# Kernel optimization log

Hardware: AMD Instinct MI355X
Metric: run time of the kernel (lower is better)

## Reference

```python
import jax, jax.numpy as jnp
import numpy as np

N_NODES, N_EDGES, N_FEAT = 50000, 500000, 128
HID, LAT, N_GRAPHS = 256, 64, 512
HEADS, DH = 8, 32  # GAT: 8 heads x 32 = 256
EPS = 1e-5


def _seg_softmax(logits, seg, num):
    m = jax.ops.segment_max(logits, seg, num_segments=num)
    m = jnp.where(jnp.isfinite(m), m, 0.0)
    e = jnp.exp(logits - m[seg])
    s = jax.ops.segment_sum(e, seg, num_segments=num)
    return e / jnp.maximum(s[seg], 1e-16)


def _bn(h, g, b):  # BatchNorm1d, batch statistics
    mu = h.mean(0)
    var = h.var(0)
    return (h - mu) * jax.lax.rsqrt(var + EPS) * g + b


def _ln(h, g, b):
    mu = h.mean(-1, keepdims=True)
    var = h.var(-1, keepdims=True)
    return (h - mu) * jax.lax.rsqrt(var + EPS) * g + b


def setup_inputs() -> dict:
    key = jax.random.key(0)
    ks = iter(jax.random.split(key, 40))
    f = lambda *s: jax.random.normal(next(ks), s, dtype=jnp.float32) * 0.05
    inp = {
        'x': jax.random.normal(next(ks), (N_NODES, N_FEAT), dtype=jnp.float32),
        'W_emb': f(N_FEAT, HID), 'b_emb': f(HID),
        'W_gcn': f(HID, HID), 'b_gcn': f(HID),
        'W_gat': f(HID, HID), 'a_src': f(HEADS, DH), 'a_dst': f(HEADS, DH), 'b_gat': f(HID),
        'W_l': f(HID, HID), 'b_l': f(HID), 'W_r': f(HID, HID),
        'bn_gamma': jnp.ones((3, HID), jnp.float32), 'bn_beta': jnp.zeros((3, HID), jnp.float32),
        'Wg1': f(HID, HID // 2), 'bg1': f(HID // 2), 'Wg2': f(HID // 2, 1), 'bg2': f(1),
        'Wm1': f(HID, HID), 'bm1': f(HID), 'ln_m_g': jnp.ones(HID, jnp.float32), 'ln_m_b': jnp.zeros(HID, jnp.float32),
        'Wm2': f(HID, LAT), 'bm2': f(LAT),
        'Wv1': f(HID, HID), 'bv1': f(HID), 'ln_v_g': jnp.ones(HID, jnp.float32), 'ln_v_b': jnp.zeros(HID, jnp.float32),
        'Wv2': f(HID, LAT), 'bv2': f(LAT),
        'edge_index': jax.random.randint(next(ks), (2, N_EDGES), 0, N_NODES, dtype=jnp.int64),
        'batch': jnp.sort(jax.random.randint(next(ks), (N_NODES,), 0, N_GRAPHS, dtype=jnp.int64)),
    }
    return inp


def _forward(x, W_emb, b_emb, W_gcn, b_gcn, W_gat, a_src, a_dst, b_gat,
             W_l, b_l, W_r, bn_gamma, bn_beta, Wg1, bg1, Wg2, bg2,
             Wm1, bm1, ln_m_g, ln_m_b, Wm2, bm2, Wv1, bv1, ln_v_g, ln_v_b, Wv2, bv2,
             edge_index, batch):
    N = x.shape[0]
    loops = jnp.arange(N)
    src_sl = jnp.concatenate([edge_index[0], loops])  # with self-loops (GCN/GAT)
    dst_sl = jnp.concatenate([edge_index[1], loops])

    h = x @ W_emb + b_emb  # [N, HID]

    # --- layer 0: GCNConv ---
    deg = jax.ops.segment_sum(jnp.ones_like(dst_sl, dtype=h.dtype), dst_sl, num_segments=N)
    dis = jax.lax.rsqrt(deg)
    norm = dis[src_sl] * dis[dst_sl]  # [E+N]
    xt = h @ W_gcn
    out = jax.ops.segment_sum(xt[src_sl] * norm[:, None], dst_sl, num_segments=N) + b_gcn
    out = jax.nn.relu(_bn(out, bn_gamma[0], bn_beta[0]))
    h = h + out

    # --- layer 1: GATConv (8 heads, concat) ---
    xt = (h @ W_gat).reshape(N, HEADS, DH)
    al_src = (xt * a_src).sum(-1)  # [N, H]
    al_dst = (xt * a_dst).sum(-1)
    logits = jax.nn.leaky_relu(al_src[src_sl] + al_dst[dst_sl], 0.2)  # [E+N, H]
    alpha = _seg_softmax(logits, dst_sl, N)
    out = jax.ops.segment_sum(xt[src_sl] * alpha[:, :, None], dst_sl, num_segments=N)
    out = out.reshape(N, HID) + b_gat
    out = jax.nn.relu(_bn(out, bn_gamma[1], bn_beta[1]))
    h = h + out

    # --- layer 2: SAGEConv (mean aggregation, no self-loops) ---
    src, dst = edge_index[0], edge_index[1]
    cnt = jax.ops.segment_sum(jnp.ones_like(dst, dtype=h.dtype), dst, num_segments=N)
    nb_mean = jax.ops.segment_sum(h[src], dst, num_segments=N) / jnp.maximum(cnt, 1.0)[:, None]
    out = nb_mean @ W_l + b_l + h @ W_r
    out = jax.nn.relu(_bn(out, bn_gamma[2], bn_beta[2]))
    h = h + out

    # --- GlobalAttention pooling ---
    gate = (jax.nn.relu(h @ Wg1 + bg1) @ Wg2 + bg2)[:, 0]  # [N]
    w = _seg_softmax(gate, batch, N_GRAPHS)
    h_graph = jax.ops.segment_sum(h * w[:, None], batch, num_segments=N_GRAPHS)  # [G, HID]

    mu = jax.nn.relu(_ln(h_graph @ Wm1 + bm1, ln_m_g, ln_m_b)) @ Wm2 + bm2
    logvar = jax.nn.relu(_ln(h_graph @ Wv1 + bv1, ln_v_g, ln_v_b)) @ Wv2 + bv2
    return mu, logvar


def reference(x, W_emb, b_emb, W_gcn, b_gcn, W_gat, a_src, a_dst, b_gat,
              W_l, b_l, W_r, bn_gamma, bn_beta, Wg1, bg1, Wg2, bg2,
              Wm1, bm1, ln_m_g, ln_m_b, Wm2, bm2, Wv1, bv1, ln_v_g, ln_v_b, Wv2, bv2,
              edge_index, batch):
    return _forward(x, W_emb, b_emb, W_gcn, b_gcn, W_gat, a_src, a_dst, b_gat,
                    W_l, b_l, W_r, bn_gamma, bn_beta, Wg1, bg1, Wg2, bg2,
                    Wm1, bm1, ln_m_g, ln_m_b, Wm2, bm2, Wv1, bv1, ln_v_g, ln_v_b, Wv2, bv2,
                    edge_index, batch)
```

## Files before the change

### kernel.cpp

```cpp
#include <hip/hip_runtime.h>
#include <cstdint>
#include <cstddef>

#define N_NODES 50000
#define N_EDGES 500000
#define NG 512
#define HID 256
#define EPS 1e-5f
#define SCB 49

typedef __attribute__((ext_vector_type(8))) __bf16 bf16x8;
typedef __attribute__((ext_vector_type(8))) ushort u16x8;
typedef __attribute__((ext_vector_type(4))) float f32x4;

__device__ __forceinline__ ushort f2bf(float f) {
  uint32_t u = __float_as_uint(f);
  uint32_t r = (u + 0x7fffu + ((u >> 16) & 1u)) >> 16;
  return (ushort)r;
}
__device__ __forceinline__ float bfu(ushort u) { return __uint_as_float(((uint32_t)u) << 16); }
__device__ __forceinline__ float4 bf4(ushort4 u) {
  return make_float4(bfu(u.x), bfu(u.y), bfu(u.z), bfu(u.w));
}

__global__ void k_csr_count(const int* __restrict__ ei, int* __restrict__ cnt) {
  int e = blockIdx.x * 256 + threadIdx.x;
  if (e < N_EDGES) atomicAdd(&cnt[ei[N_EDGES + e]], 1);
}

__global__ void k_scan_part(const int* __restrict__ cnt, int* __restrict__ psum) {
  __shared__ int red[256];
  int tid = threadIdx.x;
  int i0 = blockIdx.x * 1024 + tid * 4;
  int s = 0;
  if (i0 + 4 <= N_NODES) {
    int4 v = *reinterpret_cast<const int4*>(cnt + i0);
    s = v.x + v.y + v.z + v.w;
  } else {
    for (int k = 0; k < 4; k++)
      if (i0 + k < N_NODES) s += cnt[i0 + k];
  }
  red[tid] = s;
  __syncthreads();
  for (int o = 128; o > 0; o >>= 1) {
    if (tid < o) red[tid] += red[tid + o];
    __syncthreads();
  }
  if (tid == 0) psum[blockIdx.x] = red[0];
}

__global__ void k_scan_top(const int* __restrict__ psum, int* __restrict__ boff,
                           int* __restrict__ row_ptr) {
  int t = threadIdx.x;
  int v = (t < SCB) ? psum[t] : 0;
  int own = v;
  for (int o = 1; o < 64; o <<= 1) {
    int u = __shfl_up(v, o);
    if (t >= o) v += u;
  }
  if (t < SCB) boff[t] = v - own;
  if (t == 63) row_ptr[N_NODES] = v;
}

__global__ void k_scan_out(const int* __restrict__ cnt, const int* __restrict__ boff,
                           int* __restrict__ row_ptr, float* __restrict__ dis) {
  __shared__ int ps[256];
  int tid = threadIdx.x;
  int i0 = blockIdx.x * 1024 + tid * 4;
  int v[4];
#pragma unroll
  for (int k = 0; k < 4; k++) v[k] = (i0 + k < N_NODES) ? cnt[i0 + k] : 0;
  int s = v[0] + v[1] + v[2] + v[3];
  ps[tid] = s;
  __syncthreads();
  for (int o = 1; o < 256; o <<= 1) {
    int add = (tid >= o) ? ps[tid - o] : 0;
    __syncthreads();
    ps[tid] += add;
    __syncthreads();
  }
  int run = boff[blockIdx.x] + ((tid > 0) ? ps[tid - 1] : 0);
#pragma unroll
  for (int k = 0; k < 4; k++) {
    if (i0 + k < N_NODES) {
      row_ptr[i0 + k] = run;
      dis[i0 + k] = rsqrtf((float)v[k] + 1.0f);
      run += v[k];
    }
  }
}

__global__ void k_csr_fill(const int* __restrict__ ei, const int* __restrict__ row_ptr,
                           int* __restrict__ fill, int* __restrict__ col_src) {
  int e = blockIdx.x * 256 + threadIdx.x;
  if (e >= N_EDGES) return;
  int s = ei[e], d = ei[N_EDGES + e];
  int pos = row_ptr[d] + atomicAdd(&fill[d], 1);
  col_src[pos] = s;
}

struct WtArgs {
  const float* src[6];
  ushort* dst[6];
  int K[6];
  int C[6];
  int off[6];
};

__global__ void k_wt_all(WtArgs a) {
  int b = blockIdx.x;
  int ji = 0;
#pragma unroll
  for (int t = 1; t < 6; t++)
    if (b >= a.off[t]) ji = t;
  int K = a.K[ji], C = a.C[ji];
  int i = (b - a.off[ji]) * 256 + threadIdx.x;
  int c = i / K, k = i - c * K;
  a.dst[ji][i] = f2bf(a.src[ji][k * C + c]);
}

template <int K, int C, bool DUAL, bool AFP32, bool GATE, bool GATAL, bool BNF>
__global__ __launch_bounds__(512) void k_mgemm(
    const void* __restrict__ A1v, const ushort* __restrict__ W1t,
    const ushort* __restrict__ A2, const ushort* __restrict__ W2t,
    const float* __restrict__ bias, ushort* __restrict__ out_bf,
    const float* __restrict__ gw, const float* __restrict__ gb,
    float* __restrict__ gate, const float* __restrict__ asv,
    const float* __restrict__ adv, float* __restrict__ als,
    float* __restrict__ ald, const float* __restrict__ scsh,
    ushort* __restrict__ hbuf, int M, int relu) {
  constexpr int KS = K / 32;
  constexpr int CHK = K / 8;
  constexpr int NPAN = C / 64;
  constexpr int NISS = (64 * CHK) / 512;
  constexpr int NTOT = NPAN * (DUAL ? 2 : 1);
  constexpr int PELEM = 64 * K;
  __shared__ ushort wlds[2 * PELEM];
  const int tid = threadIdx.x;
  const int lane = tid & 63;
  const int wid = tid >> 6;
  const int r16 = lane & 15;
  const int kg = lane >> 4;
  const int rbase = blockIdx.x * 128 + wid * 16;

  const bool avalid = (rbase + r16) < M;
  int arow = rbase + r16;
  if (arow >= M) arow = M - 1;

  bf16x8 af[KS], af2[KS];
  if constexpr (BNF) {
    const ushort* xp = (const ushort*)A1v + (size_t)arow * K + kg * 8;
    ushort* hp = hbuf + (size_t)arow * K + kg * 8;
#pragma unroll
    for (int ks = 0; ks < KS; ks++) {
      int col = kg * 8 + ks * 32;
      u16x8 xv = *reinterpret_cast<const u16x8*>(xp + ks * 32);
      u16x8 hv = *reinterpret_cast<const u16x8*>(hp + ks * 32);
      float4 sc0 = *reinterpret_cast<const float4*>(scsh + col);
      float4 sc1 = *reinterpret_cast<const float4*>(scsh + col + 4);
      float4 sh0 = *reinterpret_cast<const float4*>(scsh + 256 + col);
      float4 sh1 = *reinterpret_cast<const float4*>(scsh + 256 + col + 4);
      float scv[8] = {sc0.x, sc0.y, sc0.z, sc0.w, sc1.x, sc1.y, sc1.z, sc1.w};
      float shv[8] = {sh0.x, sh0.y, sh0.z, sh0.w, sh1.x, sh1.y, sh1.z, sh1.w};
      union { u16x8 u; bf16x8 b; } cv;
#pragma unroll
      for (int j = 0; j < 8; j++) {
        float v = fmaf(bfu(xv[j]), scv[j], shv[j]);
        float hn = bfu(hv[j]) + fmaxf(v, 0.f);
        cv.u[j] = f2bf(hn);
      }
      af[ks] = cv.b;
      if (avalid) *reinterpret_cast<u16x8*>(hp + ks * 32) = cv.u;
    }
  } else if constexpr (AFP32) {
    const float* ap = (const float*)A1v + (size_t)arow * K + kg * 8;
#pragma unroll
    for (int ks = 0; ks < KS; ks++) {
      float4 lo = *reinterpret_cast<const float4*>(ap + ks * 32);
      float4 hi = *reinterpret_cast<const float4*>(ap + ks * 32 + 4);
      union { u16x8 u; bf16x8 b; } cv;
      cv.u = (u16x8){f2bf(lo.x), f2bf(lo.y), f2bf(lo.z), f2bf(lo.w),
                     f2bf(hi.x), f2bf(hi.y), f2bf(hi.z), f2bf(hi.w)};
      af[ks] = cv.b;
    }
  } else {
    const ushort* ap = (const ushort*)A1v + (size_t)arow * K + kg * 8;
#pragma unroll
    for (int ks = 0; ks < KS; ks++)
      af[ks] = *reinterpret_cast<const bf16x8*>(ap + ks * 32);
  }
  if constexpr (DUAL) {
    const ushort* ap = A2 + (size_t)arow * K + kg * 8;
#pragma unroll
    for (int ks = 0; ks < KS; ks++)
      af2[ks] = *reinterpret_cast<const bf16x8*>(ap + ks * 32);
  }

  float greg[4] = {0.f, 0.f, 0.f, 0.f};
  f32x4 acc[4];

#define STAGE_ASYNC(WSRC, PAN, BUF)                                            \
  {                                                                            \
    const ushort* base_ = (WSRC) + (size_t)((PAN) * 64) * K;                   \
    _Pragma("unroll") for (int j = 0; j < NISS; j++) {                         \
      int p_ = j * 512 + tid;                                                  \
      int c_ = p_ / CHK, jj_ = p_ % CHK;                                       \
      const ushort* g_ = base_ + c_ * K + (jj_ ^ (c_ & 7)) * 8;                \
      ushort* l_ = &wlds[(BUF) * PELEM + (j * 512 + wid * 64) * 8];            \
      __builtin_amdgcn_global_load_lds(                                        \
          (const __attribute__((address_space(1))) void*)(g_),                 \
          (__attribute__((address_space(3))) void*)(l_), 16, 0, 0);            \
    }                                                                          \
  }

#define COMPUTE(AF, BUF)                                                       \
  {                                                                            \
    const ushort* wb_ = &wlds[(BUF) * PELEM];                                  \
    _Pragma("unroll") for (int ct = 0; ct < 4; ct++) {                         \
      bf16x8 wf[KS];                                                           \
      int colr = ct * 16 + r16;                                                \
      _Pragma("unroll") for (int ks = 0; ks < KS; ks++) {                      \
        int slot = colr * CHK + ((ks * 4 + kg) ^ (r16 & 7));                   \
        wf[ks] = *reinterpret_cast<const bf16x8*>(&wb_[slot * 8]);             \
      }                                                                        \
      _Pragma("unroll") for (int ks = 0; ks < KS; ks++)                        \
        acc[ct] = __builtin_amdgcn_mfma_f32_16x16x32_bf16((AF)[ks], wf[ks],    \
                                                          acc[ct], 0, 0, 0);   \
    }                                                                          \
  }

  STAGE_ASYNC(W1t, 0, 0);
  __syncthreads();

#pragma unroll
  for (int q = 0; q < NTOT; q++) {
    const int pan = DUAL ? (q >> 1) : q;
    const int pass = DUAL ? (q & 1) : 0;
    const int cur = q & 1;
    const int c0 = pan * 64;
    if (pass == 0) {
#pragma unroll
      for (int ct = 0; ct < 4; ct++) acc[ct] = (f32x4){0.f, 0.f, 0.f, 0.f};
    }
    if (q + 1 < NTOT) {
      const int npan = DUAL ? ((q + 1) >> 1) : (q + 1);
      const ushort* Wq = (DUAL && ((q + 1) & 1)) ? W2t : W1t;
      STAGE_ASYNC(Wq, npan, cur ^ 1);
    }
    if (DUAL && pass) {
      COMPUTE(af2, cur);
    } else {
      COMPUTE(af, cur);
    }
    if (pass == (DUAL ? 1 : 0)) {
      if constexpr (GATE) {
#pragma unroll
        for (int ct = 0; ct < 4; ct++) {
          int col = c0 + ct * 16 + r16;
          float bv = bias[col];
          float wv = gw[col];
#pragma unroll
          for (int i = 0; i < 4; i++) {
            float v = fmaxf(acc[ct][i] + bv, 0.f);
            greg[i] = fmaf(v, wv, greg[i]);
          }
        }
      } else {
#pragma unroll
        for (int ct = 0; ct < 4; ct++) {
          int col = c0 + ct * 16 + r16;
          float bv = bias ? bias[col] : 0.f;
#pragma unroll
          for (int i = 0; i < 4; i++) {
            int row = rbase + kg * 4 + i;
            if (row < M) {
              float v = acc[ct][i] + bv;
              if (relu) v = fmaxf(v, 0.f);
              out_bf[(size_t)row * C + col] = f2bf(v);
            }
          }
        }
      }
      if constexpr (GATAL) {
        float ps_[2][4], pd_[2][4];
#pragma unroll
        for (int h2 = 0; h2 < 2; h2++)
#pragma unroll
          for (int i = 0; i < 4; i++) { ps_[h2][i] = 0.f; pd_[h2][i] = 0.f; }
#pragma unroll
        for (int ct = 0; ct < 4; ct++) {
          int col = c0 + ct * 16 + r16;
          float as_ = asv[col], ad_ = adv[col];
          int h2 = ct >> 1;
#pragma unroll
          for (int i = 0; i < 4; i++) {
            ps_[h2][i] = fmaf(acc[ct][i], as_, ps_[h2][i]);
            pd_[h2][i] = fmaf(acc[ct][i], ad_, pd_[h2][i]);
          }
        }
#pragma unroll
        for (int h2 = 0; h2 < 2; h2++)
#pragma unroll
          for (int i = 0; i < 4; i++) {
#pragma unroll
            for (int o = 1; o < 16; o <<= 1) {
              ps_[h2][i] += __shfl_xor(ps_[h2][i], o);
              pd_[h2][i] += __shfl_xor(pd_[h2][i], o);
            }
          }
        if (r16 == 0) {
#pragma unroll
          for (int i = 0; i < 4; i++) {
            int row = rbase + kg * 4 + i;
            if (row < M) {
              als[row * 8 + pan * 2 + 0] = ps_[0][i];
              ald[row * 8 + pan * 2 + 0] = pd_[0][i];
              als[row * 8 + pan * 2 + 1] = ps_[1][i];
              ald[row * 8 + pan * 2 + 1] = pd_[1][i];
            }
          }
        }
      }
    }
    __syncthreads();
  }

  if constexpr (GATE) {
#pragma unroll
    for (int i = 0; i < 4; i++) {
#pragma unroll
      for (int o = 1; o < 16; o <<= 1) greg[i] += __shfl_xor(greg[i], o);
    }
    if (r16 == 0) {
      float b0 = gb[0];
#pragma unroll
      for (int i = 0; i < 4; i++) {
        int row = rbase + kg * 4 + i;
        if (row < M) gate[row] = greg[i] + b0;
      }
    }
  }
#undef STAGE_ASYNC
#undef COMPUTE
}

__global__ void k_gcn_agg(const ushort* __restrict__ xt, const float* __restrict__ dis,
                          const int* __restrict__ row_ptr, const int* __restrict__ col_src,
                          const float* __restrict__ b_gcn, ushort* __restrict__ outb) {
  int node = blockIdx.x * 4 + (threadIdx.x >> 6);
  if (node >= N_NODES) return;
  int lane = threadIdx.x & 63;
  int half = lane >> 5;
  int c0 = (lane & 31) * 8;
  float di = dis[node];
  float acc[8];
#pragma unroll
  for (int j = 0; j < 8; j++) acc[j] = 0.f;
  int b = row_ptr[node], e = row_ptr[node + 1];
  int g0 = b;
  for (; g0 + 8 <= e; g0 += 8) {
    int i0 = g0 + half * 4;
    int s0 = col_src[i0], s1 = col_src[i0 + 1], s2 = col_src[i0 + 2], s3 = col_src[i0 + 3];
    float w0 = di * dis[s0], w1 = di * dis[s1], w2 = di * dis[s2], w3 = di * dis[s3];
    u16x8 u0 = *reinterpret_cast<const u16x8*>(xt + (size_t)s0 * HID + c0);
    u16x8 u1 = *reinterpret_cast<const u16x8*>(xt + (size_t)s1 * HID + c0);
    u16x8 u2 = *reinterpret_cast<const u16x8*>(xt + (size_t)s2 * HID + c0);
    u16x8 u3 = *reinterpret_cast<const u16x8*>(xt + (size_t)s3 * HID + c0);
#pragma unroll
    for (int j = 0; j < 8; j++) {
      acc[j] = fmaf(bfu(u0[j]), w0, acc[j]);
      acc[j] = fmaf(bfu(u1[j]), w1, acc[j]);
      acc[j] = fmaf(bfu(u2[j]), w2, acc[j]);
      acc[j] = fmaf(bfu(u3[j]), w3, acc[j]);
    }
  }
  for (; g0 + 4 <= e; g0 += 4) {
    int i0 = g0 + half * 2;
    int s0 = col_src[i0], s1 = col_src[i0 + 1];
    float w0 = di * dis[s0], w1 = di * dis[s1];
    u16x8 u0 = *reinterpret_cast<const u16x8*>(xt + (size_t)s0 * HID + c0);
    u16x8 u1 = *reinterpret_cast<const u16x8*>(xt + (size_t)s1 * HID + c0);
#pragma unroll
    for (int j = 0; j < 8; j++) {
      acc[j] = fmaf(bfu(u0[j]), w0, acc[j]);
      acc[j] = fmaf(bfu(u1[j]), w1, acc[j]);
    }
  }
  {
    int i0 = g0 + half * 2;
    int s0 = 0, s1 = 0;
    float w0 = 0.f, w1 = 0.f;
    if (i0 < e) { s0 = col_src[i0]; w0 = di * dis[s0]; }
    if (i0 + 1 < e) { s1 = col_src[i0 + 1]; w1 = di * dis[s1]; }
    u16x8 u0 = *reinterpret_cast<const u16x8*>(xt + (size_t)s0 * HID + c0);
    u16x8 u1 = *reinterpret_cast<const u16x8*>(xt + (size_t)s1 * HID + c0);
#pragma unroll
    for (int j = 0; j < 8; j++) {
      acc[j] = fmaf(bfu(u0[j]), w0, acc[j]);
      acc[j] = fmaf(bfu(u1[j]), w1, acc[j]);
    }
  }
#pragma unroll
  for (int j = 0; j < 8; j++) acc[j] += __shfl_xor(acc[j], 32);
  if (!half) {
    u16x8 un = *reinterpret_cast<const u16x8*>(xt + (size_t)node * HID + c0);
    float w0 = di * di;
    u16x8 r;
#pragma unroll
    for (int j = 0; j < 8; j++) {
      float v = fmaf(bfu(un[j]), w0, acc[j]) + b_gcn[c0 + j];
      r[j] = f2bf(v);
    }
    *reinterpret_cast<u16x8*>(outb + (size_t)node * HID + c0) = r;
  }
}

__device__ __forceinline__ float leaky02(float x) { return x > 0.f ? x : 0.2f * x; }

__global__ void k_gat_agg(const ushort* __restrict__ xt, const float* __restrict__ alsrc,
                          const float* __restrict__ aldst, const int* __restrict__ row_ptr,
                          const int* __restrict__ col_src, const float* __restrict__ b_gat,
                          ushort* __restrict__ outb) {
  int node = blockIdx.x * 4 + (threadIdx.x >> 6);
  if (node >= N_NODES) return;
  int lane = threadIdx.x & 63;
  int half = lane >> 5;
  int l32 = lane & 31;
  int c0 = l32 * 8;
  int hh = l32 >> 2;
  float ad = aldst[node * 8 + hh];
  float acc[8];
#pragma unroll
  for (int j = 0; j < 8; j++) acc[j] = 0.f;
  float s = 0.f;
  int b = row_ptr[node], e = row_ptr[node + 1];
  int g0 = b;
  for (; g0 + 8 <= e; g0 += 8) {
    int i0 = g0 + half * 4;
    int s0 = col_src[i0], s1 = col_src[i0 + 1], s2 = col_src[i0 + 2], s3 = col_src[i0 + 3];
    float g0v = alsrc[s0 * 8 + hh], g1v = alsrc[s1 * 8 + hh];
    float g2v = alsrc[s2 * 8 + hh], g3v = alsrc[s3 * 8 + hh];
    u16x8 u0 = *reinterpret_cast<const u16x8*>(xt + (size_t)s0 * HID + c0);
    u16x8 u1 = *reinterpret_cast<const u16x8*>(xt + (size_t)s1 * HID + c0);
    u16x8 u2 = *reinterpret_cast<const u16x8*>(xt + (size_t)s2 * HID + c0);
    u16x8 u3 = *reinterpret_cast<const u16x8*>(xt + (size_t)s3 * HID + c0);
    float a0 = __expf(leaky02(g0v + ad));
    float a1 = __expf(leaky02(g1v + ad));
    float a2 = __expf(leaky02(g2v + ad));
    float a3 = __expf(leaky02(g3v + ad));
    s += a0 + a1 + a2 + a3;
#pragma unroll
    for (int j = 0; j < 8; j++) {
      acc[j] = fmaf(bfu(u0[j]), a0, acc[j]);
      acc[j] = fmaf(bfu(u1[j]), a1, acc[j]);
      acc[j] = fmaf(bfu(u2[j]), a2, acc[j]);
      acc[j] = fmaf(bfu(u3[j]), a3, acc[j]);
    }
  }
  for (; g0 + 4 <= e; g0 += 4) {
    int i0 = g0 + half * 2;
    int s0 = col_src[i0], s1 = col_src[i0 + 1];
    float a0 = __expf(leaky02(alsrc[s0 * 8 + hh] + ad));
    float a1 = __expf(leaky02(alsrc[s1 * 8 + hh] + ad));
    u16x8 u0 = *reinterpret_cast<const u16x8*>(xt + (size_t)s0 * HID + c0);
    u16x8 u1 = *reinterpret_cast<const u16x8*>(xt + (size_t)s1 * HID + c0);
    s += a0 + a1;
#pragma unroll
    for (int j = 0; j < 8; j++) {
      acc[j] = fmaf(bfu(u0[j]), a0, acc[j]);
      acc[j] = fmaf(bfu(u1[j]), a1, acc[j]);
    }
  }
  {
    int i0 = g0 + half * 2;
    int s0 = 0, s1 = 0;
    float a0 = 0.f, a1 = 0.f;
    if (i0 < e) { s0 = col_src[i0]; a0 = __expf(leaky02(alsrc[s0 * 8 + hh] + ad)); }
    if (i0 + 1 < e) { s1 = col_src[i0 + 1]; a1 = __expf(leaky02(alsrc[s1 * 8 + hh] + ad)); }
    u16x8 u0 = *reinterpret_cast<const u16x8*>(xt + (size_t)s0 * HID + c0);
    u16x8 u1 = *reinterpret_cast<const u16x8*>(xt + (size_t)s1 * HID + c0);
    s += a0 + a1;
#pragma unroll
    for (int j = 0; j < 8; j++) {
      acc[j] = fmaf(bfu(u0[j]), a0, acc[j]);
      acc[j] = fmaf(bfu(u1[j]), a1, acc[j]);
    }
  }
#pragma unroll
  for (int j = 0; j < 8; j++) acc[j] += __shfl_xor(acc[j], 32);
  s += __shfl_xor(s, 32);
  if (!half) {
    float e0 = __expf(leaky02(alsrc[node * 8 + hh] + ad));
    u16x8 un = *reinterpret_cast<const u16x8*>(xt + (size_t)node * HID + c0);
    float inv_s = 1.0f / (s + e0);
    u16x8 r;
#pragma unroll
    for (int j = 0; j < 8; j++) {
      float v = fmaf(bfu(un[j]), e0, acc[j]) * inv_s + b_gat[c0 + j];
      r[j] = f2bf(v);
    }
    *reinterpret_cast<u16x8*>(outb + (size_t)node * HID + c0) = r;
  }
}

__global__ void k_sage_agg(const ushort* __restrict__ h, const int* __restrict__ row_ptr,
                           const int* __restrict__ col_src, ushort* __restrict__ outb) {
  int node = blockIdx.x * 4 + (threadIdx.x >> 6);
  if (node >= N_NODES) return;
  int lane = threadIdx.x & 63;
  int half = lane >> 5;
  int c0 = (lane & 31) * 8;
  float acc[8];
#pragma unroll
  for (int j = 0; j < 8; j++) acc[j] = 0.f;
  int b = row_ptr[node], e = row_ptr[node + 1];
  int g0 = b;
  for (; g0 + 8 <= e; g0 += 8) {
    int i0 = g0 + half * 4;
    int s0 = col_src[i0], s1 = col_src[i0 + 1], s2 = col_src[i0 + 2], s3 = col_src[i0 + 3];
    u16x8 u0 = *reinterpret_cast<const u16x8*>(h + (size_t)s0 * HID + c0);
    u16x8 u1 = *reinterpret_cast<const u16x8*>(h + (size_t)s1 * HID + c0);
    u16x8 u2 = *reinterpret_cast<const u16x8*>(h + (size_t)s2 * HID + c0);
    u16x8 u3 = *reinterpret_cast<const u16x8*>(h + (size_t)s3 * HID + c0);
#pragma unroll
    for (int j = 0; j < 8; j++)
      acc[j] += (bfu(u0[j]) + bfu(u1[j])) + (bfu(u2[j]) + bfu(u3[j]));
  }
  for (; g0 + 4 <= e; g0 += 4) {
    int i0 = g0 + half * 2;
    int s0 = col_src[i0], s1 = col_src[i0 + 1];
    u16x8 u0 = *reinterpret_cast<const u16x8*>(h + (size_t)s0 * HID + c0);
    u16x8 u1 = *reinterpret_cast<const u16x8*>(h + (size_t)s1 * HID + c0);
#pragma unroll
    for (int j = 0; j < 8; j++) acc[j] += bfu(u0[j]) + bfu(u1[j]);
  }
  {
    int i0 = g0 + half * 2;
    int s0 = 0, s1 = 0;
    float w0 = 0.f, w1 = 0.f;
    if (i0 < e) { s0 = col_src[i0]; w0 = 1.f; }
    if (i0 + 1 < e) { s1 = col_src[i0 + 1]; w1 = 1.f; }
    u16x8 u0 = *reinterpret_cast<const u16x8*>(h + (size_t)s0 * HID + c0);
    u16x8 u1 = *reinterpret_cast<const u16x8*>(h + (size_t)s1 * HID + c0);
#pragma unroll
    for (int j = 0; j < 8; j++) {
      acc[j] = fmaf(bfu(u0[j]), w0, acc[j]);
      acc[j] = fmaf(bfu(u1[j]), w1, acc[j]);
    }
  }
#pragma unroll
  for (int j = 0; j < 8; j++) acc[j] += __shfl_xor(acc[j], 32);
  if (!half) {
    float inv = 1.0f / fmaxf((float)(e - b), 1.0f);
    u16x8 r;
#pragma unroll
    for (int j = 0; j < 8; j++) r[j] = f2bf(acc[j] * inv);
    *reinterpret_cast<u16x8*>(outb + (size_t)node * HID + c0) = r;
  }
}

__global__ __launch_bounds__(256) void k_bn_stats(const ushort* __restrict__ x,
                                                  float* __restrict__ stats) {
  int tid = threadIdx.x;
  int cg = tid & 31;
  int rs = tid >> 5;
  int c0 = cg * 8;
  float s[8], q[8];
#pragma unroll
  for (int j = 0; j < 8; j++) { s[j] = 0.f; q[j] = 0.f; }
  for (int r = blockIdx.x * 8 + rs; r < N_NODES; r += gridDim.x * 8) {
    u16x8 v = *reinterpret_cast<const u16x8*>(x + (size_t)r * HID + c0);
#pragma unroll
    for (int j = 0; j < 8; j++) {
      float f = bfu(v[j]);
      s[j] += f;
      q[j] = fmaf(f, f, q[j]);
    }
  }
  __shared__ float ls[512];
  ls[tid] = 0.f;
  ls[tid + 256] = 0.f;
  __syncthreads();
#pragma unroll
  for (int j = 0; j < 8; j++) {
    atomicAdd(&ls[c0 + j], s[j]);
    atomicAdd(&ls[256 + c0 + j], q[j]);
  }
  __syncthreads();
  atomicAdd(&stats[tid], ls[tid]);
  atomicAdd(&stats[tid + 256], ls[tid + 256]);
}

__global__ void k_bn_coef(const float* __restrict__ stats, const float* __restrict__ gamma,
                          const float* __restrict__ beta, float* __restrict__ scsh) {
  int c = threadIdx.x;
  const float invN = 1.0f / (float)N_NODES;
  float mu = stats[c] * invN;
  float var = stats[256 + c] * invN - mu * mu;
  float sc = gamma[c] * rsqrtf(var + EPS);
  scsh[c] = sc;
  scsh[256 + c] = beta[c] - mu * sc;
}

__global__ void k_bn_apply(const ushort* __restrict__ x, const float* __restrict__ scsh,
                           ushort* __restrict__ h_bf) {
  int total = N_NODES * 64;
  for (int i = blockIdx.x * 256 + threadIdx.x; i < total; i += gridDim.x * 256) {
    int c4 = (i & 63) * 4;
    float4 xv = bf4(*reinterpret_cast<const ushort4*>(x + (size_t)i * 4));
    float4 sc = *reinterpret_cast<const float4*>(scsh + c4);
    float4 sh = *reinterpret_cast<const float4*>(scsh + 256 + c4);
    float4 hv = bf4(*reinterpret_cast<const ushort4*>(h_bf + (size_t)i * 4));
    hv.x += fmaxf(fmaf(xv.x, sc.x, sh.x), 0.f);
    hv.y += fmaxf(fmaf(xv.y, sc.y, sh.y), 0.f);
    hv.z += fmaxf(fmaf(xv.z, sc.z, sh.z), 0.f);
    hv.w += fmaxf(fmaf(xv.w, sc.w, sh.w), 0.f);
    *reinterpret_cast<ushort4*>(h_bf + (size_t)i * 4) =
        make_ushort4(f2bf(hv.x), f2bf(hv.y), f2bf(hv.z), f2bf(hv.w));
  }
}

__global__ void k_gstart(const int* __restrict__ batch, int* __restrict__ gstart) {
  int g = blockIdx.x * 256 + threadIdx.x;
  if (g > NG) return;
  int lo = 0, hi = N_NODES;
  while (lo < hi) {
    int mid = (lo + hi) >> 1;
    if (batch[mid] < g) lo = mid + 1; else hi = mid;
  }
  gstart[g] = lo;
}

__global__ void k_pool(const ushort* __restrict__ hb, const float* __restrict__ gate,
                       const int* __restrict__ gstart, float* __restrict__ hg) {
  __shared__ float red[256];
  __shared__ float wbuf[256];
  int g = blockIdx.x, tid = threadIdx.x;
  int b = gstart[g], e = gstart[g + 1];
  float m = -1e30f;
  for (int r = b + tid; r < e; r += 256) m = fmaxf(m, gate[r]);
  red[tid] = m;
  __syncthreads();
  for (int o = 128; o > 0; o >>= 1) {
    if (tid < o) red[tid] = fmaxf(red[tid], red[tid + o]);
    __syncthreads();
  }
  m = red[0];
  __syncthreads();
  float s = 0.f;
  for (int r = b + tid; r < e; r += 256) s += __expf(gate[r] - m);
  red[tid] = s;
  __syncthreads();
  for (int o = 128; o > 0; o >>= 1) {
    if (tid < o) red[tid] += red[tid + o];
    __syncthreads();
  }
  float inv = 1.0f / fmaxf(red[0], 1e-16f);
  __syncthreads();
  float acc = 0.f;
  for (int cb = b; cb < e; cb += 256) {
    int r = cb + tid;
    wbuf[tid] = (r < e) ? __expf(gate[r] - m) : 0.f;
    __syncthreads();
    int n = min(256, e - cb);
    for (int j = 0; j < n; j++)
      acc = fmaf(bfu(hb[(size_t)(cb + j) * HID + tid]), wbuf[j], acc);
    __syncthreads();
  }
  hg[(size_t)g * HID + tid] = acc * inv;
}

__global__ void k_mlp(const float* __restrict__ hg, const float* __restrict__ W1,
                      const float* __restrict__ b1, const float* __restrict__ lng,
                      const float* __restrict__ lnb, const float* __restrict__ W2,
                      const float* __restrict__ b2, float* __restrict__ out) {
  __shared__ float row[HID];
  __shared__ float z[HID];
  __shared__ float red[HID];
  int g = blockIdx.x, tid = threadIdx.x;
  row[tid] = hg[(size_t)g * HID + tid];
  __syncthreads();
  float acc = b1[tid];
  for (int k = 0; k < HID; k++) acc = fmaf(row[k], W1[(size_t)k * HID + tid], acc);
  red[tid] = acc;
  __syncthreads();
  for (int o = 128; o > 0; o >>= 1) {
    if (tid < o) red[tid] += red[tid + o];
    __syncthreads();
  }
  float mu = red[0] * (1.0f / HID);
  __syncthreads();
  red[tid] = acc * acc;
  __syncthreads();
  for (int o = 128; o > 0; o >>= 1) {
    if (tid < o) red[tid] += red[tid + o];
    __syncthreads();
  }
  float var = red[0] * (1.0f / HID) - mu * mu;
  float zz = (acc - mu) * rsqrtf(var + EPS) * lng[tid] + lnb[tid];
  z[tid] = fmaxf(zz, 0.f);
  __syncthreads();
  if (tid < 64) {
    float o = b2[tid];
    for (int k = 0; k < HID; k++) o = fmaf(z[k], W2[(size_t)k * 64 + tid], o);
    out[(size_t)g * 64 + tid] = o;
  }
}

extern "C" void kernel_launch(void* const* d_in, const int* in_sizes, int n_in,
                              void* d_out, int out_size, void* d_ws, size_t ws_size,
                              hipStream_t stream) {
  const float* x     = (const float*)d_in[0];
  const float* W_emb = (const float*)d_in[1];
  const float* b_emb = (const float*)d_in[2];
  const float* W_gcn = (const float*)d_in[3];
  const float* b_gcn = (const float*)d_in[4];
  const float* W_gat = (const float*)d_in[5];
  const float* a_src = (const float*)d_in[6];
  const float* a_dst = (const float*)d_in[7];
  const float* b_gat = (const float*)d_in[8];
  const float* W_l   = (const float*)d_in[9];
  const float* b_l   = (const float*)d_in[10];
  const float* W_r   = (const float*)d_in[11];
  const float* bn_g  = (const float*)d_in[12];
  const float* bn_b  = (const float*)d_in[13];
  const float* Wg1   = (const float*)d_in[14];
  const float* bg1   = (const float*)d_in[15];
  const float* Wg2   = (const float*)d_in[16];
  const float* bg2   = (const float*)d_in[17];
  const float* Wm1   = (const float*)d_in[18];
  const float* bm1   = (const float*)d_in[19];
  const float* lnmg  = (const float*)d_in[20];
  const float* lnmb  = (const float*)d_in[21];
  const float* Wm2   = (const float*)d_in[22];
  const float* bm2   = (const float*)d_in[23];
  const float* Wv1   = (const float*)d_in[24];
  const float* bv1   = (const float*)d_in[25];
  const float* lnvg  = (const float*)d_in[26];
  const float* lnvb  = (const float*)d_in[27];
  const float* Wv2   = (const float*)d_in[28];
  const float* bv2   = (const float*)d_in[29];
  const int* ei      = (const int*)d_in[30];
  const int* batch   = (const int*)d_in[31];
  float* out = (float*)d_out;

  float* ws = (float*)d_ws;
  float* h     = ws;
  float* t1    = h + (size_t)N_NODES * HID;
  float* alsrc = t1 + (size_t)N_NODES * HID;
  float* aldst = alsrc + N_NODES * 8;
  float* dis   = aldst + N_NODES * 8;
  float* gate  = dis + N_NODES;
  float* hg    = gate + N_NODES;
  float* zbase = hg + NG * HID;
  float* bnst  = zbase;
  int* row_cnt = (int*)(zbase + 3 * 512);
  int* fill    = row_cnt + N_NODES;
  int* row_ptr = fill + N_NODES;
  int* col_src = row_ptr + N_NODES + 1;
  int* gstart  = col_src + N_EDGES;
  int* psum    = gstart + NG + 1;
  int* boff    = psum + 64;
  float* scsh  = (float*)(boff + 64);

  ushort* t1b = (ushort*)t1;

  size_t off = (size_t)((char*)(scsh + 3 * 512) - (char*)d_ws);
  off = (off + 15) & ~(size_t)15;
  ushort* h_bf   = (ushort*)((char*)d_ws + off);
  ushort* t0_bf  = h_bf + (size_t)N_NODES * HID;
  ushort* wemb_t = t0_bf + (size_t)N_NODES * HID;
  ushort* wgcn_t = wemb_t + 128 * 256;
  ushort* wgat_t = wgcn_t + 256 * 256;
  ushort* wr_t   = wgat_t + 256 * 256;
  ushort* wl_t   = wr_t + 256 * 256;
  ushort* wg1_t  = wl_t + 256 * 256;

  size_t zbytes = (size_t)3 * 512 * 4 + 2 * (size_t)N_NODES * 4;
  hipMemsetAsync(zbase, 0, zbytes, stream);

  k_csr_count<<<(N_EDGES + 255) / 256, 256, 0, stream>>>(ei, row_cnt);
  k_scan_part<<<SCB, 256, 0, stream>>>(row_cnt, psum);
  k_scan_top<<<1, 64, 0, stream>>>(psum, boff, row_ptr);
  k_scan_out<<<SCB, 256, 0, stream>>>(row_cnt, boff, row_ptr, dis);
  k_csr_fill<<<(N_EDGES + 255) / 256, 256, 0, stream>>>(ei, row_ptr, fill, col_src);

  WtArgs wa;
  wa.src[0] = W_emb; wa.dst[0] = wemb_t; wa.K[0] = 128; wa.C[0] = 256; wa.off[0] = 0;
  wa.src[1] = W_gcn; wa.dst[1] = wgcn_t; wa.K[1] = 256; wa.C[1] = 256; wa.off[1] = 128;
  wa.src[2] = W_gat; wa.dst[2] = wgat_t; wa.K[2] = 256; wa.C[2] = 256; wa.off[2] = 384;
  wa.src[3] = W_r;   wa.dst[3] = wr_t;   wa.K[3] = 256; wa.C[3] = 256; wa.off[3] = 640;
  wa.src[4] = W_l;   wa.dst[4] = wl_t;   wa.K[4] = 256; wa.C[4] = 256; wa.off[4] = 896;
  wa.src[5] = Wg1;   wa.dst[5] = wg1_t;  wa.K[5] = 256; wa.C[5] = 128; wa.off[5] = 1152;
  k_wt_all<<<1280, 256, 0, stream>>>(wa);

  const int RB = (N_NODES + 127) / 128;
  const int AB = (N_NODES + 3) / 4;

  k_mgemm<128, 256, false, true, false, false, false><<<RB, 512, 0, stream>>>(
      x, wemb_t, nullptr, nullptr, b_emb, h_bf, nullptr, nullptr, nullptr,
      nullptr, nullptr, nullptr, nullptr, nullptr, nullptr, N_NODES, 0);

  k_mgemm<256, 256, false, false, false, false, false><<<RB, 512, 0, stream>>>(
      h_bf, wgcn_t, nullptr, nullptr, nullptr, t0_bf, nullptr, nullptr, nullptr,
      nullptr, nullptr, nullptr, nullptr, nullptr, nullptr, N_NODES, 0);
  k_gcn_agg<<<AB, 256, 0, stream>>>(t0_bf, dis, row_ptr, col_src, b_gcn, t1b);
  k_bn_stats<<<1024, 256, 0, stream>>>(t1b, bnst);
  k_bn_coef<<<1, 256, 0, stream>>>(bnst, bn_g, bn_b, scsh);

  k_mgemm<256, 256, false, false, false, true, true><<<RB, 512, 0, stream>>>(
      t1b, wgat_t, nullptr, nullptr, nullptr, t0_bf, nullptr, nullptr, nullptr,
      a_src, a_dst, alsrc, aldst, scsh, h_bf, N_NODES, 0);
  k_gat_agg<<<AB, 256, 0, stream>>>(t0_bf, alsrc, aldst, row_ptr, col_src, b_gat, t1b);
  k_bn_stats<<<1024, 256, 0, stream>>>(t1b, bnst + 512);
  k_bn_coef<<<1, 256, 0, stream>>>(bnst + 512, bn_g + HID, bn_b + HID, scsh + 512);
  k_bn_apply<<<1024, 256, 0, stream>>>(t1b, scsh + 512, h_bf);

  k_sage_agg<<<AB, 256, 0, stream>>>(h_bf, row_ptr, col_src, t0_bf);
  k_mgemm<256, 256, true, false, false, false, false><<<RB, 512, 0, stream>>>(
      h_bf, wr_t, t0_bf, wl_t, b_l, t1b, nullptr, nullptr, nullptr,
      nullptr, nullptr, nullptr, nullptr, nullptr, nullptr, N_NODES, 0);
  k_bn_stats<<<1024, 256, 0, stream>>>(t1b, bnst + 1024);
  k_bn_coef<<<1, 256, 0, stream>>>(bnst + 1024, bn_g + 2 * HID, bn_b + 2 * HID, scsh + 1024);

  k_mgemm<256, 128, false, false, true, false, true><<<RB, 512, 0, stream>>>(
      t1b, wg1_t, nullptr, nullptr, bg1, nullptr, Wg2, bg2, gate,
      nullptr, nullptr, nullptr, nullptr, scsh + 1024, h_bf, N_NODES, 1);
  k_gstart<<<3, 256, 0, stream>>>(batch, gstart);
  k_pool<<<NG, 256, 0, stream>>>(h_bf, gate, gstart, hg);

  k_mlp<<<NG, 256, 0, stream>>>(hg, Wm1, bm1, lnmg, lnmb, Wm2, bm2, out);
  k_mlp<<<NG, 256, 0, stream>>>(hg, Wv1, bv1, lnvg, lnvb, Wv2, bv2, out + (size_t)NG * 64);
}
```

Baseline: 549.4 us.

## Halve GEMM row tile and K-split weight panels; store GAT logits head-major

Result: no change. 550.6 us (+0.2%).

```diff
diff --git a/kernel.cpp b/kernel.cpp
--- a/kernel.cpp
+++ b/kernel.cpp
@@ -120,7 +120,7 @@
 }
 
 template <int K, int C, bool DUAL, bool AFP32, bool GATE, bool GATAL, bool BNF>
-__global__ __launch_bounds__(512) void k_mgemm(
+__global__ __launch_bounds__(256) void k_mgemm(
     const void* __restrict__ A1v, const ushort* __restrict__ W1t,
     const ushort* __restrict__ A2, const ushort* __restrict__ W2t,
     const float* __restrict__ bias, ushort* __restrict__ out_bf,
@@ -130,18 +130,21 @@
     float* __restrict__ ald, const float* __restrict__ scsh,
     ushort* __restrict__ hbuf, int M, int relu) {
   constexpr int KS = K / 32;
-  constexpr int CHK = K / 8;
+  constexpr int KSH = KS / 2;
+  constexpr int KHALF = K / 2;
+  constexpr int CHKH = KHALF / 8;
   constexpr int NPAN = C / 64;
-  constexpr int NISS = (64 * CHK) / 512;
-  constexpr int NTOT = NPAN * (DUAL ? 2 : 1);
-  constexpr int PELEM = 64 * K;
+  constexpr int LOWB = DUAL ? 4 : 2;
+  constexpr int NTOT = NPAN * LOWB;
+  constexpr int NISS = (64 * CHKH) / 256;
+  constexpr int PELEM = 64 * KHALF;
   __shared__ ushort wlds[2 * PELEM];
   const int tid = threadIdx.x;
   const int lane = tid & 63;
   const int wid = tid >> 6;
   const int r16 = lane & 15;
   const int kg = lane >> 4;
-  const int rbase = blockIdx.x * 128 + wid * 16;
+  const int rbase = blockIdx.x * 64 + wid * 16;
 
   const bool avalid = (rbase + r16) < M;
   int arow = rbase + r16;
@@ -199,60 +202,64 @@
   float greg[4] = {0.f, 0.f, 0.f, 0.f};
   f32x4 acc[4];
 
-#define STAGE_ASYNC(WSRC, PAN, BUF)                                            \
+#define STAGE_ASYNC(WSRC, PAN, KH, BUF)                                        \
   {                                                                            \
-    const ushort* base_ = (WSRC) + (size_t)((PAN) * 64) * K;                   \
+    const ushort* base_ = (WSRC) + (size_t)((PAN) * 64) * K + (KH) * KHALF;    \
     _Pragma("unroll") for (int j = 0; j < NISS; j++) {                         \
-      int p_ = j * 512 + tid;                                                  \
-      int c_ = p_ / CHK, jj_ = p_ % CHK;                                       \
+      int p_ = j * 256 + tid;                                                  \
+      int c_ = p_ / CHKH, jj_ = p_ % CHKH;                                     \
       const ushort* g_ = base_ + c_ * K + (jj_ ^ (c_ & 7)) * 8;                \
-      ushort* l_ = &wlds[(BUF) * PELEM + (j * 512 + wid * 64) * 8];            \
+      ushort* l_ = &wlds[(BUF) * PELEM + (j * 256 + wid * 64) * 8];            \
       __builtin_amdgcn_global_load_lds(                                        \
           (const __attribute__((address_space(1))) void*)(g_),                 \
           (__attribute__((address_space(3))) void*)(l_), 16, 0, 0);            \
     }                                                                          \
   }
 
-#define COMPUTE(AF, BUF)                                                       \
+#define COMPUTE(AF, KH, BUF)                                                   \
   {                                                                            \
     const ushort* wb_ = &wlds[(BUF) * PELEM];                                  \
     _Pragma("unroll") for (int ct = 0; ct < 4; ct++) {                         \
-      bf16x8 wf[KS];                                                           \
+      bf16x8 wf[KSH];                                                          \
       int colr = ct * 16 + r16;                                                \
-      _Pragma("unroll") for (int ks = 0; ks < KS; ks++) {                      \
-        int slot = colr * CHK + ((ks * 4 + kg) ^ (r16 & 7));                   \
-        wf[ks] = *reinterpret_cast<const bf16x8*>(&wb_[slot * 8]);             \
+      _Pragma("unroll") for (int ksl = 0; ksl < KSH; ksl++) {                  \
+        int slot = colr * CHKH + ((ksl * 4 + kg) ^ (r16 & 7));                 \
+        wf[ksl] = *reinterpret_cast<const bf16x8*>(&wb_[slot * 8]);            \
       }                                                                        \
-      _Pragma("unroll") for (int ks = 0; ks < KS; ks++)                        \
-        acc[ct] = __builtin_amdgcn_mfma_f32_16x16x32_bf16((AF)[ks], wf[ks],    \
-                                                          acc[ct], 0, 0, 0);   \
+      _Pragma("unroll") for (int ksl = 0; ksl < KSH; ksl++)                    \
+        acc[ct] = __builtin_amdgcn_mfma_f32_16x16x32_bf16(                     \
+            (AF)[(KH) * KSH + ksl], wf[ksl], acc[ct], 0, 0, 0);                \
     }                                                                          \
   }
 
-  STAGE_ASYNC(W1t, 0, 0);
+  STAGE_ASYNC(W1t, 0, 0, 0);
   __syncthreads();
 
 #pragma unroll
   for (int q = 0; q < NTOT; q++) {
-    const int pan = DUAL ? (q >> 1) : q;
-    const int pass = DUAL ? (q & 1) : 0;
-    const int cur = q & 1;
+    const int kh = q & 1;
+    const int pass = DUAL ? ((q >> 1) & 1) : 0;
+    const int pan = DUAL ? (q >> 2) : (q >> 1);
+    const int cur = q & 1 ? 1 : 0;
+    const int bufq = q & 1;
     const int c0 = pan * 64;
-    if (pass == 0) {
+    if ((q & (LOWB - 1)) == 0) {
 #pragma unroll
       for (int ct = 0; ct < 4; ct++) acc[ct] = (f32x4){0.f, 0.f, 0.f, 0.f};
     }
     if (q + 1 < NTOT) {
-      const int npan = DUAL ? ((q + 1) >> 1) : (q + 1);
-      const ushort* Wq = (DUAL && ((q + 1) & 1)) ? W2t : W1t;
-      STAGE_ASYNC(Wq, npan, cur ^ 1);
+      const int nkh = (q + 1) & 1;
+      const int npass = DUAL ? (((q + 1) >> 1) & 1) : 0;
+      const int npan = DUAL ? ((q + 1) >> 2) : ((q + 1) >> 1);
+      const ushort* Wq = (DUAL && npass) ? W2t : W1t;
+      STAGE_ASYNC(Wq, npan, nkh, bufq ^ 1);
     }
     if (DUAL && pass) {
-      COMPUTE(af2, cur);
+      COMPUTE(af2, kh, bufq);
     } else {
-      COMPUTE(af, cur);
-    }
-    if (pass == (DUAL ? 1 : 0)) {
+      COMPUTE(af, kh, bufq);
+    }
+    if ((q & (LOWB - 1)) == (LOWB - 1)) {
       if constexpr (GATE) {
 #pragma unroll
         for (int ct = 0; ct < 4; ct++) {
@@ -310,13 +317,15 @@
           }
         if (r16 == 0) {
 #pragma unroll
-          for (int i = 0; i < 4; i++) {
-            int row = rbase + kg * 4 + i;
-            if (row < M) {
-              als[row * 8 + pan * 2 + 0] = ps_[0][i];
-              ald[row * 8 + pan * 2 + 0] = pd_[0][i];
-              als[row * 8 + pan * 2 + 1] = ps_[1][i];
-              ald[row * 8 + pan * 2 + 1] = pd_[1][i];
+          for (int h2 = 0; h2 < 2; h2++) {
+            int head = pan * 2 + h2;
+#pragma unroll
+            for (int i = 0; i < 4; i++) {
+              int row = rbase + kg * 4 + i;
+              if (row < M) {
+                als[(size_t)head * N_NODES + row] = ps_[h2][i];
+                ald[(size_t)head * N_NODES + row] = pd_[h2][i];
+              }
             }
           }
         }
@@ -428,7 +437,8 @@
   int l32 = lane & 31;
   int c0 = l32 * 8;
   int hh = l32 >> 2;
-  float ad = aldst[node * 8 + hh];
+  const float* alh = alsrc + (size_t)hh * N_NODES;
+  float ad = aldst[(size_t)hh * N_NODES + node];
   float acc[8];
 #pragma unroll
   for (int j = 0; j < 8; j++) acc[j] = 0.f;
@@ -438,8 +448,7 @@
   for (; g0 + 8 <= e; g0 += 8) {
     int i0 = g0 + half * 4;
     int s0 = col_src[i0], s1 = col_src[i0 + 1], s2 = col_src[i0 + 2], s3 = col_src[i0 + 3];
-    float g0v = alsrc[s0 * 8 + hh], g1v = alsrc[s1 * 8 + hh];
-    float g2v = alsrc[s2 * 8 + hh], g3v = alsrc[s3 * 8 + hh];
+    float g0v = alh[s0], g1v = alh[s1], g2v = alh[s2], g3v = alh[s3];
     u16x8 u0 = *reinterpret_cast<const u16x8*>(xt + (size_t)s0 * HID + c0);
     u16x8 u1 = *reinterpret_cast<const u16x8*>(xt + (size_t)s1 * HID + c0);
     u16x8 u2 = *reinterpret_cast<const u16x8*>(xt + (size_t)s2 * HID + c0);
@@ -460,8 +469,8 @@
   for (; g0 + 4 <= e; g0 += 4) {
     int i0 = g0 + half * 2;
     int s0 = col_src[i0], s1 = col_src[i0 + 1];
-    float a0 = __expf(leaky02(alsrc[s0 * 8 + hh] + ad));
-    float a1 = __expf(leaky02(alsrc[s1 * 8 + hh] + ad));
+    float a0 = __expf(leaky02(alh[s0] + ad));
+    float a1 = __expf(leaky02(alh[s1] + ad));
     u16x8 u0 = *reinterpret_cast<const u16x8*>(xt + (size_t)s0 * HID + c0);
     u16x8 u1 = *reinterpret_cast<const u16x8*>(xt + (size_t)s1 * HID + c0);
     s += a0 + a1;
@@ -475,8 +484,8 @@
     int i0 = g0 + half * 2;
     int s0 = 0, s1 = 0;
     float a0 = 0.f, a1 = 0.f;
-    if (i0 < e) { s0 = col_src[i0]; a0 = __expf(leaky02(alsrc[s0 * 8 + hh] + ad)); }
-    if (i0 + 1 < e) { s1 = col_src[i0 + 1]; a1 = __expf(leaky02(alsrc[s1 * 8 + hh] + ad)); }
+    if (i0 < e) { s0 = col_src[i0]; a0 = __expf(leaky02(alh[s0] + ad)); }
+    if (i0 + 1 < e) { s1 = col_src[i0 + 1]; a1 = __expf(leaky02(alh[s1] + ad)); }
     u16x8 u0 = *reinterpret_cast<const u16x8*>(xt + (size_t)s0 * HID + c0);
     u16x8 u1 = *reinterpret_cast<const u16x8*>(xt + (size_t)s1 * HID + c0);
     s += a0 + a1;
@@ -490,7 +499,7 @@
   for (int j = 0; j < 8; j++) acc[j] += __shfl_xor(acc[j], 32);
   s += __shfl_xor(s, 32);
   if (!half) {
-    float e0 = __expf(leaky02(alsrc[node * 8 + hh] + ad));
+    float e0 = __expf(leaky02(alh[node] + ad));
     u16x8 un = *reinterpret_cast<const u16x8*>(xt + (size_t)node * HID + c0);
     float inv_s = 1.0f / (s + e0);
     u16x8 r;
@@ -794,21 +803,21 @@
   wa.src[5] = Wg1;   wa.dst[5] = wg1_t;  wa.K[5] = 256; wa.C[5] = 128; wa.off[5] = 1152;
   k_wt_all<<<1280, 256, 0, stream>>>(wa);
 
-  const int RB = (N_NODES + 127) / 128;
+  const int RB = (N_NODES + 63) / 64;
   const int AB = (N_NODES + 3) / 4;
 
-  k_mgemm<128, 256, false, true, false, false, false><<<RB, 512, 0, stream>>>(
+  k_mgemm<128, 256, false, true, false, false, false><<<RB, 256, 0, stream>>>(
       x, wemb_t, nullptr, nullptr, b_emb, h_bf, nullptr, nullptr, nullptr,
       nullptr, nullptr, nullptr, nullptr, nullptr, nullptr, N_NODES, 0);
 
-  k_mgemm<256, 256, false, false, false, false, false><<<RB, 512, 0, stream>>>(
+  k_mgemm<256, 256, false, false, false, false, false><<<RB, 256, 0, stream>>>(
       h_bf, wgcn_t, nullptr, nullptr, nullptr, t0_bf, nullptr, nullptr, nullptr,
       nullptr, nullptr, nullptr, nullptr, nullptr, nullptr, N_NODES, 0);
   k_gcn_agg<<<AB, 256, 0, stream>>>(t0_bf, dis, row_ptr, col_src, b_gcn, t1b);
   k_bn_stats<<<1024, 256, 0, stream>>>(t1b, bnst);
   k_bn_coef<<<1, 256, 0, stream>>>(bnst, bn_g, bn_b, scsh);
 
-  k_mgemm<256, 256, false, false, false, true, true><<<RB, 512, 0, stream>>>(
+  k_mgemm<256, 256, false, false, false, true, true><<<RB, 256, 0, stream>>>(
       t1b, wgat_t, nullptr, nullptr, nullptr, t0_bf, nullptr, nullptr, nullptr,
       a_src, a_dst, alsrc, aldst, scsh, h_bf, N_NODES, 0);
   k_gat_agg<<<AB, 256, 0, stream>>>(t0_bf, alsrc, aldst, row_ptr, col_src, b_gat, t1b);
@@ -817,13 +826,13 @@
   k_bn_apply<<<1024, 256, 0, stream>>>(t1b, scsh + 512, h_bf);
 
   k_sage_agg<<<AB, 256, 0, stream>>>(h_bf, row_ptr, col_src, t0_bf);
-  k_mgemm<256, 256, true, false, false, false, false><<<RB, 512, 0, stream>>>(
+  k_mgemm<256, 256, true, false, false, false, false><<<RB, 256, 0, stream>>>(
       h_bf, wr_t, t0_bf, wl_t, b_l, t1b, nullptr, nullptr, nullptr,
       nullptr, nullptr, nullptr, nullptr, nullptr, nullptr, N_NODES, 0);
   k_bn_stats<<<1024, 256, 0, stream>>>(t1b, bnst + 1024);
   k_bn_coef<<<1, 256, 0, stream>>>(bnst + 1024, bn_g + 2 * HID, bn_b + 2 * HID, scsh + 1024);
 
-  k_mgemm<256, 128, false, false, true, false, true><<<RB, 512, 0, stream>>>(
+  k_mgemm<256, 128, false, false, true, false, true><<<RB, 256, 0, stream>>>(
       t1b, wg1_t, nullptr, nullptr, bg1, nullptr, Wg2, bg2, gate,
       nullptr, nullptr, nullptr, nullptr, scsh + 1024, h_bf, N_NODES, 1);
   k_gstart<<<3, 256, 0, stream>>>(batch, gstart);
```
